# Kernel tuning notes

Hardware: AMD Instinct MI355X
Metric: run time of the kernel (lower is better)

## Reference

```python
import jax, jax.numpy as jnp
import numpy as np

E, N, D = 640000, 10000, 128  # edges, nodes, feature dim (edge=node=global=128)
H, O = 256, 128               # MLP hidden / output dims; concat dim = 4*D = 512


def setup_inputs() -> dict:
    key = jax.random.key(0)
    ks = jax.random.split(key, 7)
    return {
        "edge_attr": jax.random.normal(ks[0], (E, D), dtype=jnp.float32),
        "node_attr": jax.random.normal(ks[1], (N, D), dtype=jnp.float32),
        "global_attr": jax.random.normal(ks[2], (D,), dtype=jnp.float32),
        "senders": jax.random.randint(ks[3], (E,), 0, N),
        "receivers": jax.random.randint(ks[4], (E,), 0, N),
        "W1": jax.random.normal(ks[5], (4 * D, H), dtype=jnp.float32) / np.float32(np.sqrt(4 * D)),
        "b1": jnp.zeros((H,), dtype=jnp.float32),
        "W2": jax.random.normal(ks[6], (H, O), dtype=jnp.float32) / np.float32(np.sqrt(H)),
        "b2": jnp.zeros((O,), dtype=jnp.float32),
    }


def reference(edge_attr, node_attr, global_attr, senders, receivers, W1, b1, W2, b2):
    # Batched form of the per-edge Python loop:
    #   cat([e.data, e.receiver.data, e.sender.data, G.global_attribute.data]) -> updater MLP
    num_edges = edge_attr.shape[0]
    g = jnp.broadcast_to(global_attr, (num_edges, global_attr.shape[0]))  # [E, Dg]
    x = jnp.concatenate(
        [edge_attr, node_attr[receivers], node_attr[senders], g], axis=-1
    )  # [E, 4D]
    h = jax.nn.relu(x @ W1 + b1)  # [E, H]
    return h @ W2 + b2            # [E, O] : updated edge attributes
```

## Files before the change

### kernel.cpp

```cpp
#include <hip/hip_runtime.h>
#include <hip/hip_bf16.h>


typedef __attribute__((ext_vector_type(8))) short bf16x8;
typedef __attribute__((ext_vector_type(4))) float f32x4;
typedef __attribute__((ext_vector_type(2))) unsigned int u32x2;

static __device__ __forceinline__ unsigned short f2bf(float f) {
    unsigned u = __builtin_bit_cast(unsigned, f);
    u += 0x7FFFu + ((u >> 16) & 1u);
    return (unsigned short)(u >> 16);
}

static __device__ __forceinline__ unsigned cvt_pk_bf16(float lo, float hi) {
    unsigned r;
    asm("v_cvt_pk_bf16_f32 %0, %1, %2" : "=v"(r) : "v"(lo), "v"(hi));
    return r;
}

static __device__ __forceinline__ float bflo(unsigned u) {
    return __builtin_bit_cast(float, u << 16);
}
static __device__ __forceinline__ float bfhi(unsigned u) {
    return __builtin_bit_cast(float, u & 0xFFFF0000u);
}


__global__ void prep_w1_kernel(const float* __restrict__ W1,
                               ushort* __restrict__ w1f) {
    int id = blockIdx.x * 256 + threadIdx.x;
    if (id >= 16 * 12 * 64) return;
    int l = id & 63, blk = id >> 6;
    int ks = blk % 12, gnt = blk / 12;
    int n  = gnt * 16 + (l & 15);
    int k0 = ks * 32 + (l >> 4) * 8;
    ushort tmp[8];
    #pragma unroll
    for (int j = 0; j < 8; ++j) tmp[j] = f2bf(W1[(k0 + j) * 256 + n]);
    *(bf16x8*)&w1f[(size_t)id * 8] = *(bf16x8*)tmp;
}

__global__ void prep_w2_kernel(const float* __restrict__ W2,
                               ushort* __restrict__ w2f) {
    int id = blockIdx.x * 256 + threadIdx.x;
    if (id >= 8 * 8 * 64) return;
    int l = id & 63, blk = id >> 6;
    int ks = blk % 8, gnt = blk / 8;
    int n  = gnt * 16 + (l & 15);
    int k0 = ks * 32 + (l >> 4) * 8;
    ushort tmp[8];
    #pragma unroll
    for (int j = 0; j < 8; ++j) tmp[j] = f2bf(W2[(k0 + j) * 128 + n]);
    *(bf16x8*)&w2f[(size_t)id * 8] = *(bf16x8*)tmp;
}

__global__ void prep_hbias_kernel(const float* __restrict__ W1,
                                  const float* __restrict__ b1,
                                  const float* __restrict__ g,
                                  float* __restrict__ hbias) {
    int n = threadIdx.x;
    float acc = b1[n];
    for (int k = 0; k < 128; ++k) acc += g[k] * W1[(384 + k) * 256 + n];
    hbias[n] = acc;
}

__global__ __launch_bounds__(256) void prep_proj_kernel(
    const float* __restrict__ node_attr,
    const ushort* __restrict__ w1f,
    const float* __restrict__ hbias,
    ushort* __restrict__ Pr,
    ushort* __restrict__ Ps)
{
    __shared__ ushort Xn[64 * 128];

    const int t = threadIdx.x, l = t & 63, wn = t >> 6;
    const int base = blockIdx.x * 64;
    const int lr = l & 15, q = l >> 4, lk = q * 8;

    #pragma unroll
    for (int p = 0; p < 4; ++p) {
        int chunk = p * 256 + t;
        int r  = chunk >> 4;
        int c0 = (chunk & 15) * 8;
        int node = base + r; if (node >= 10000) node = 9999;
        const float4* src = (const float4*)(node_attr + (size_t)node * 128 + c0);
        float4 a = src[0];
        float4 b = src[1];
        uint4 uu = { cvt_pk_bf16(a.x, a.y), cvt_pk_bf16(a.z, a.w),
                     cvt_pk_bf16(b.x, b.y), cvt_pk_bf16(b.z, b.w) };
        *(bf16x8*)&Xn[r * 128 + (c0 ^ ((r & 7) << 3))] = __builtin_bit_cast(bf16x8, uu);
    }
    __syncthreads();

    #pragma unroll
    for (int s = 0; s < 2; ++s) {
        f32x4 acc[4][4];
        #pragma unroll
        for (int mt = 0; mt < 4; ++mt)
            #pragma unroll
            for (int nt = 0; nt < 4; ++nt)
                acc[mt][nt] = (f32x4){0.f, 0.f, 0.f, 0.f};

        #pragma unroll
        for (int ks = 0; ks < 4; ++ks) {
            bf16x8 B[4];
            #pragma unroll
            for (int nt = 0; nt < 4; ++nt)
                B[nt] = *(const bf16x8*)&w1f[
                    (size_t)(((wn * 4 + nt) * 12 + 4 + s * 4 + ks) * 64 + l) * 8];
            bf16x8 X[4];
            const int kk = ks * 32 + lk;
            #pragma unroll
            for (int mt = 0; mt < 4; ++mt) {
                const int row = mt * 16 + lr;
                X[mt] = *(const bf16x8*)&Xn[row * 128 + (kk ^ ((row & 7) << 3))];
            }
            #pragma unroll
            for (int mt = 0; mt < 4; ++mt)
                #pragma unroll
                for (int nt = 0; nt < 4; ++nt)
                    acc[mt][nt] = __builtin_amdgcn_mfma_f32_16x16x32_bf16(
                        B[nt], X[mt], acc[mt][nt], 0, 0, 0);
        }

        ushort* P = s ? Ps : Pr;
        #pragma unroll
        for (int nt = 0; nt < 4; ++nt) {
            const int F = wn * 64 + nt * 16 + q * 4;
            float4 hb4 = {0.f, 0.f, 0.f, 0.f};
            if (s == 0) hb4 = *(const float4*)&hbias[F];
            #pragma unroll
            for (int mt = 0; mt < 4; ++mt) {
                const int node = base + mt * 16 + lr;
                if (node < 10000) {
                    u32x2 w = { cvt_pk_bf16(acc[mt][nt][0] + hb4.x,
                                            acc[mt][nt][1] + hb4.y),
                                cvt_pk_bf16(acc[mt][nt][2] + hb4.z,
                                            acc[mt][nt][3] + hb4.w) };
                    *(u32x2*)&P[(size_t)node * 256 + F] = w;
                }
            }
        }
    }
}


__global__ __launch_bounds__(256, 3) void edge_mlp_kernel(
    const float* __restrict__ edge_attr,
    const int* __restrict__ senders,
    const int* __restrict__ receivers,
    const ushort* __restrict__ w1f,
    const ushort* __restrict__ w2f,
    const ushort* __restrict__ Pr,
    const ushort* __restrict__ Ps,
    const float* __restrict__ b2,
    float* __restrict__ out)
{
    __shared__ ushort Xe[64 * 128];
    __shared__ ushort Hs[64 * 256];

    const int t    = threadIdx.x;
    const int l    = t & 63;
    const int wid  = t >> 6;
    const int base = blockIdx.x * 64;

    const int lr = l & 15;
    const int q  = l >> 4;
    const int lk = q * 8;

    int pr_off[4], ps_off[4];
    #pragma unroll
    for (int mt = 0; mt < 4; ++mt) {
        int e = base + mt * 16 + lr;
        pr_off[mt] = receivers[e] * 256;
        ps_off[mt] = senders[e]   * 256;
    }

    #pragma unroll
    for (int p = 0; p < 4; ++p) {
        int chunk = p * 256 + t;
        int r  = chunk >> 4;
        int c0 = (chunk & 15) * 8;
        const float4* src = (const float4*)(edge_attr + (size_t)(base + r) * 128 + c0);
        float4 a = src[0];
        float4 b = src[1];
        uint4 uu = { cvt_pk_bf16(a.x, a.y), cvt_pk_bf16(a.z, a.w),
                     cvt_pk_bf16(b.x, b.y), cvt_pk_bf16(b.z, b.w) };
        *(bf16x8*)&Xe[r * 128 + (c0 ^ ((r & 7) << 3))] = __builtin_bit_cast(bf16x8, uu);
    }

    __syncthreads();

    f32x4 acc[4][4];
    #pragma unroll
    for (int mt = 0; mt < 4; ++mt)
        #pragma unroll
        for (int nt = 0; nt < 4; ++nt)
            acc[mt][nt] = (f32x4){0.f, 0.f, 0.f, 0.f};

    bf16x8 B[2][4];
    #pragma unroll
    for (int nt = 0; nt < 4; ++nt)
        B[0][nt] = *(const bf16x8*)&w1f[(size_t)(((wid * 4 + nt) * 12 + 0) * 64 + l) * 8];

    #pragma unroll
    for (int ks = 0; ks < 4; ++ks) {
        const int cur = ks & 1;
        if (ks < 3) {
            #pragma unroll
            for (int nt = 0; nt < 4; ++nt)
                B[cur ^ 1][nt] = *(const bf16x8*)&w1f[
                    (size_t)(((wid * 4 + nt) * 12 + (ks + 1)) * 64 + l) * 8];
        }
        bf16x8 X[4];
        const int kk = ks * 32 + lk;
        #pragma unroll
        for (int mt = 0; mt < 4; ++mt) {
            const int row = mt * 16 + lr;
            X[mt] = *(const bf16x8*)&Xe[row * 128 + (kk ^ ((row & 7) << 3))];
        }
        #pragma unroll
        for (int mt = 0; mt < 4; ++mt)
            #pragma unroll
            for (int nt = 0; nt < 4; ++nt)
                acc[mt][nt] = __builtin_amdgcn_mfma_f32_16x16x32_bf16(
                    B[cur][nt], X[mt], acc[mt][nt], 0, 0, 0);
    }

    u32x2 pg[4][4], sg[4][4];
    #pragma unroll
    for (int nt = 0; nt < 4; ++nt) {
        const int F = wid * 64 + nt * 16 + q * 4;
        #pragma unroll
        for (int mt = 0; mt < 4; ++mt) {
            pg[nt][mt] = *(const u32x2*)&Pr[pr_off[mt] + F];
            sg[nt][mt] = *(const u32x2*)&Ps[ps_off[mt] + F];
        }
    }

    #pragma unroll
    for (int nt = 0; nt < 4; ++nt) {
        const int F = wid * 64 + nt * 16 + q * 4;
        #pragma unroll
        for (int mt = 0; mt < 4; ++mt) {
            u32x2 p = pg[nt][mt], s = sg[nt][mt];
            float v0 = fmaxf(acc[mt][nt][0] + bflo(p.x) + bflo(s.x), 0.f);
            float v1 = fmaxf(acc[mt][nt][1] + bfhi(p.x) + bfhi(s.x), 0.f);
            float v2 = fmaxf(acc[mt][nt][2] + bflo(p.y) + bflo(s.y), 0.f);
            float v3 = fmaxf(acc[mt][nt][3] + bfhi(p.y) + bfhi(s.y), 0.f);
            u32x2 w = { cvt_pk_bf16(v0, v1), cvt_pk_bf16(v2, v3) };
            const int edge = mt * 16 + lr;
            *(u32x2*)&Hs[edge * 256 + (F ^ ((edge & 7) << 3))] = w;
        }
    }

    __syncthreads();

    f32x4 acc2[4][2];
    #pragma unroll
    for (int mt = 0; mt < 4; ++mt)
        #pragma unroll
        for (int nt = 0; nt < 2; ++nt)
            acc2[mt][nt] = (f32x4){0.f, 0.f, 0.f, 0.f};

    bf16x8 W2b[2][2];
    #pragma unroll
    for (int nt = 0; nt < 2; ++nt)
        W2b[0][nt] = *(const bf16x8*)&w2f[(size_t)(((wid * 2 + nt) * 8 + 0) * 64 + l) * 8];

    #pragma unroll
    for (int ks = 0; ks < 8; ++ks) {
        const int cur = ks & 1;
        if (ks < 7) {
            #pragma unroll
            for (int nt = 0; nt < 2; ++nt)
                W2b[cur ^ 1][nt] = *(const bf16x8*)&w2f[
                    (size_t)(((wid * 2 + nt) * 8 + (ks + 1)) * 64 + l) * 8];
        }
        bf16x8 Hfr[4];
        const int F = ks * 32 + lk;
        #pragma unroll
        for (int mt = 0; mt < 4; ++mt) {
            const int edge = mt * 16 + lr;
            Hfr[mt] = *(const bf16x8*)&Hs[edge * 256 + (F ^ ((edge & 7) << 3))];
        }
        #pragma unroll
        for (int mt = 0; mt < 4; ++mt)
            #pragma unroll
            for (int nt = 0; nt < 2; ++nt)
                acc2[mt][nt] = __builtin_amdgcn_mfma_f32_16x16x32_bf16(
                    W2b[cur][nt], Hfr[mt], acc2[mt][nt], 0, 0, 0);
    }

    #pragma unroll
    for (int nt = 0; nt < 2; ++nt) {
        const int F = wid * 32 + nt * 16 + q * 4;
        float4 b24 = *(const float4*)&b2[F];
        #pragma unroll
        for (int mt = 0; mt < 4; ++mt) {
            float4 o = { acc2[mt][nt][0] + b24.x, acc2[mt][nt][1] + b24.y,
                         acc2[mt][nt][2] + b24.z, acc2[mt][nt][3] + b24.w };
            *(float4*)&out[(size_t)(base + mt * 16 + lr) * 128 + F] = o;
        }
    }
}


extern "C" void kernel_launch(void* const* d_in, const int* in_sizes, int n_in,
                              void* d_out, int out_size, void* d_ws, size_t ws_size,
                              hipStream_t stream) {
    (void)in_sizes; (void)n_in; (void)out_size; (void)ws_size;

    const float* edge_attr   = (const float*)d_in[0];
    const float* node_attr   = (const float*)d_in[1];
    const float* global_attr = (const float*)d_in[2];
    const int*   senders     = (const int*)d_in[3];
    const int*   receivers   = (const int*)d_in[4];
    const float* W1          = (const float*)d_in[5];
    const float* b1          = (const float*)d_in[6];
    const float* W2          = (const float*)d_in[7];
    const float* b2          = (const float*)d_in[8];
    float* out = (float*)d_out;

    ushort* w1f   = (ushort*)d_ws;
    ushort* w2f   = (ushort*)((char*)d_ws + 196608);
    float*  hbias = (float*)((char*)d_ws + 262144);
    ushort* Pr    = (ushort*)((char*)d_ws + 263168);
    ushort* Ps    = (ushort*)((char*)d_ws + 5383168);

    hipLaunchKernelGGL(prep_w1_kernel,    dim3(48),  dim3(256), 0, stream, W1, w1f);
    hipLaunchKernelGGL(prep_w2_kernel,    dim3(16),  dim3(256), 0, stream, W2, w2f);
    hipLaunchKernelGGL(prep_hbias_kernel, dim3(1),   dim3(256), 0, stream, W1, b1, global_attr, hbias);
    hipLaunchKernelGGL(prep_proj_kernel,  dim3(157), dim3(256), 0, stream,
                       node_attr, w1f, hbias, Pr, Ps);

    hipLaunchKernelGGL(edge_mlp_kernel, dim3(10000), dim3(256), 0, stream,
                       edge_attr, senders, receivers, w1f, w2f, Pr, Ps, b2, out);
}
```

Baseline: 312.6 us.

## Make edge MLP kernel persistent with register-prefetched next-tile edge data

Replaces the one-block-per-tile launch of 10000 blocks with a persistent grid of 768 blocks looping over tiles. Each block prefetches the next tile's edge features and sender/receiver indices into registers while computing the current tile, and writes them to LDS after the first GEMM. This is meant to hide global load latency and avoid per-block startup cost. In exchange, occupancy is lowered to 2 blocks per SM and register pressure rises.

Result: slower. 596.2 us (+90.7%).

```diff
diff --git a/kernel.cpp b/kernel.cpp
--- a/kernel.cpp
+++ b/kernel.cpp
@@ -5,6 +5,9 @@
 typedef __attribute__((ext_vector_type(8))) short bf16x8;
 typedef __attribute__((ext_vector_type(4))) float f32x4;
 typedef __attribute__((ext_vector_type(2))) unsigned int u32x2;
+
+#define NTILE 10000
+#define GRID  768
 
 static __device__ __forceinline__ unsigned short f2bf(float f) {
     unsigned u = __builtin_bit_cast(unsigned, f);
@@ -23,6 +26,13 @@
 }
 static __device__ __forceinline__ float bfhi(unsigned u) {
     return __builtin_bit_cast(float, u & 0xFFFF0000u);
+}
+
+static __device__ __forceinline__ void block_sync_lds() {
+    __builtin_amdgcn_sched_barrier(0);
+    asm volatile("s_waitcnt lgkmcnt(0)" ::: "memory");
+    __builtin_amdgcn_s_barrier();
+    __builtin_amdgcn_sched_barrier(0);
 }
 
 
@@ -82,7 +92,7 @@
         int chunk = p * 256 + t;
         int r  = chunk >> 4;
         int c0 = (chunk & 15) * 8;
-        int node = base + r; if (node >= 10000) node = 9999;
+        int node = base + r; if (node >= NTILE) node = NTILE - 1;
         const float4* src = (const float4*)(node_attr + (size_t)node * 128 + c0);
         float4 a = src[0];
         float4 b = src[1];
@@ -132,7 +142,7 @@
             #pragma unroll
             for (int mt = 0; mt < 4; ++mt) {
                 const int node = base + mt * 16 + lr;
-                if (node < 10000) {
+                if (node < NTILE) {
                     u32x2 w = { cvt_pk_bf16(acc[mt][nt][0] + hb4.x,
                                             acc[mt][nt][1] + hb4.y),
                                 cvt_pk_bf16(acc[mt][nt][2] + hb4.z,
@@ -145,7 +155,7 @@
 }
 
 
-__global__ __launch_bounds__(256, 3) void edge_mlp_kernel(
+__global__ __launch_bounds__(256, 2) void edge_mlp_kernel(
     const float* __restrict__ edge_attr,
     const int* __restrict__ senders,
     const int* __restrict__ receivers,
@@ -162,146 +172,197 @@
     const int t    = threadIdx.x;
     const int l    = t & 63;
     const int wid  = t >> 6;
-    const int base = blockIdx.x * 64;
-
     const int lr = l & 15;
     const int q  = l >> 4;
     const int lk = q * 8;
 
-    int pr_off[4], ps_off[4];
-    #pragma unroll
-    for (int mt = 0; mt < 4; ++mt) {
-        int e = base + mt * 16 + lr;
-        pr_off[mt] = receivers[e] * 256;
-        ps_off[mt] = senders[e]   * 256;
-    }
-
+    int sr[4], sc[4];
     #pragma unroll
     for (int p = 0; p < 4; ++p) {
         int chunk = p * 256 + t;
-        int r  = chunk >> 4;
-        int c0 = (chunk & 15) * 8;
-        const float4* src = (const float4*)(edge_attr + (size_t)(base + r) * 128 + c0);
-        float4 a = src[0];
-        float4 b = src[1];
-        uint4 uu = { cvt_pk_bf16(a.x, a.y), cvt_pk_bf16(a.z, a.w),
-                     cvt_pk_bf16(b.x, b.y), cvt_pk_bf16(b.z, b.w) };
-        *(bf16x8*)&Xe[r * 128 + (c0 ^ ((r & 7) << 3))] = __builtin_bit_cast(bf16x8, uu);
-    }
-
-    __syncthreads();
-
-    f32x4 acc[4][4];
-    #pragma unroll
-    for (int mt = 0; mt < 4; ++mt)
+        sr[p] = chunk >> 4;
+        sc[p] = (chunk & 15) * 8;
+    }
+
+    int ti = blockIdx.x;
+
+    int recvC[4], sendC[4], recvN[4], sendN[4];
+    #pragma unroll
+    for (int mt = 0; mt < 4; ++mt) {
+        int e = ti * 64 + mt * 16 + lr;
+        recvC[mt] = receivers[e];
+        sendC[mt] = senders[e];
+    }
+
+    float4 er[8];
+    #pragma unroll
+    for (int p = 0; p < 4; ++p) {
+        const float4* src = (const float4*)(edge_attr + (size_t)(ti * 64 + sr[p]) * 128 + sc[p]);
+        er[2 * p]     = src[0];
+        er[2 * p + 1] = src[1];
+    }
+    #pragma unroll
+    for (int p = 0; p < 4; ++p) {
+        uint4 uu = { cvt_pk_bf16(er[2*p].x, er[2*p].y),  cvt_pk_bf16(er[2*p].z, er[2*p].w),
+                     cvt_pk_bf16(er[2*p+1].x, er[2*p+1].y), cvt_pk_bf16(er[2*p+1].z, er[2*p+1].w) };
+        *(bf16x8*)&Xe[sr[p] * 128 + (sc[p] ^ ((sr[p] & 7) << 3))] = __builtin_bit_cast(bf16x8, uu);
+    }
+
+    int tn = ti + GRID; if (tn >= NTILE) tn = ti;
+    #pragma unroll
+    for (int p = 0; p < 4; ++p) {
+        const float4* src = (const float4*)(edge_attr + (size_t)(tn * 64 + sr[p]) * 128 + sc[p]);
+        er[2 * p]     = src[0];
+        er[2 * p + 1] = src[1];
+    }
+    #pragma unroll
+    for (int mt = 0; mt < 4; ++mt) {
+        int e = tn * 64 + mt * 16 + lr;
+        recvN[mt] = receivers[e];
+        sendN[mt] = senders[e];
+    }
+
+    block_sync_lds();
+
+    for (; ti < NTILE; ti += GRID) {
+        u32x2 pg[4][4], sg[4][4];
+        #pragma unroll
+        for (int nt = 0; nt < 4; ++nt) {
+            const int F = wid * 64 + nt * 16 + q * 4;
+            #pragma unroll
+            for (int mt = 0; mt < 4; ++mt) {
+                pg[nt][mt] = *(const u32x2*)&Pr[(size_t)recvC[mt] * 256 + F];
+                sg[nt][mt] = *(const u32x2*)&Ps[(size_t)sendC[mt] * 256 + F];
+            }
+        }
+
+        f32x4 acc[4][4];
+        #pragma unroll
+        for (int mt = 0; mt < 4; ++mt)
+            #pragma unroll
+            for (int nt = 0; nt < 4; ++nt)
+                acc[mt][nt] = (f32x4){0.f, 0.f, 0.f, 0.f};
+
+        bf16x8 B[2][4];
         #pragma unroll
         for (int nt = 0; nt < 4; ++nt)
-            acc[mt][nt] = (f32x4){0.f, 0.f, 0.f, 0.f};
-
-    bf16x8 B[2][4];
-    #pragma unroll
-    for (int nt = 0; nt < 4; ++nt)
-        B[0][nt] = *(const bf16x8*)&w1f[(size_t)(((wid * 4 + nt) * 12 + 0) * 64 + l) * 8];
-
-    #pragma unroll
-    for (int ks = 0; ks < 4; ++ks) {
-        const int cur = ks & 1;
-        if (ks < 3) {
-            #pragma unroll
-            for (int nt = 0; nt < 4; ++nt)
-                B[cur ^ 1][nt] = *(const bf16x8*)&w1f[
-                    (size_t)(((wid * 4 + nt) * 12 + (ks + 1)) * 64 + l) * 8];
-        }
-        bf16x8 X[4];
-        const int kk = ks * 32 + lk;
+            B[0][nt] = *(const bf16x8*)&w1f[(size_t)(((wid * 4 + nt) * 12 + 0) * 64 + l) * 8];
+
+        #pragma unroll
+        for (int ks = 0; ks < 4; ++ks) {
+            const int cur = ks & 1;
+            if (ks < 3) {
+                #pragma unroll
+                for (int nt = 0; nt < 4; ++nt)
+                    B[cur ^ 1][nt] = *(const bf16x8*)&w1f[
+                        (size_t)(((wid * 4 + nt) * 12 + (ks + 1)) * 64 + l) * 8];
+            }
+            bf16x8 X[4];
+            const int kk = ks * 32 + lk;
+            #pragma unroll
+            for (int mt = 0; mt < 4; ++mt) {
+                const int row = mt * 16 + lr;
+                X[mt] = *(const bf16x8*)&Xe[row * 128 + (kk ^ ((row & 7) << 3))];
+            }
+            #pragma unroll
+            for (int mt = 0; mt < 4; ++mt)
+                #pragma unroll
+                for (int nt = 0; nt < 4; ++nt)
+                    acc[mt][nt] = __builtin_amdgcn_mfma_f32_16x16x32_bf16(
+                        B[cur][nt], X[mt], acc[mt][nt], 0, 0, 0);
+        }
+
+        #pragma unroll
+        for (int nt = 0; nt < 4; ++nt) {
+            const int F = wid * 64 + nt * 16 + q * 4;
+            #pragma unroll
+            for (int mt = 0; mt < 4; ++mt) {
+                u32x2 p = pg[nt][mt], s = sg[nt][mt];
+                float v0 = fmaxf(acc[mt][nt][0] + bflo(p.x) + bflo(s.x), 0.f);
+                float v1 = fmaxf(acc[mt][nt][1] + bfhi(p.x) + bfhi(s.x), 0.f);
+                float v2 = fmaxf(acc[mt][nt][2] + bflo(p.y) + bflo(s.y), 0.f);
+                float v3 = fmaxf(acc[mt][nt][3] + bfhi(p.y) + bfhi(s.y), 0.f);
+                u32x2 w = { cvt_pk_bf16(v0, v1), cvt_pk_bf16(v2, v3) };
+                const int edge = mt * 16 + lr;
+                *(u32x2*)&Hs[edge * 256 + (F ^ ((edge & 7) << 3))] = w;
+            }
+        }
+
+        block_sync_lds();
+
+        #pragma unroll
+        for (int p = 0; p < 4; ++p) {
+            uint4 uu = { cvt_pk_bf16(er[2*p].x, er[2*p].y),  cvt_pk_bf16(er[2*p].z, er[2*p].w),
+                         cvt_pk_bf16(er[2*p+1].x, er[2*p+1].y), cvt_pk_bf16(er[2*p+1].z, er[2*p+1].w) };
+            *(bf16x8*)&Xe[sr[p] * 128 + (sc[p] ^ ((sr[p] & 7) << 3))] = __builtin_bit_cast(bf16x8, uu);
+        }
+
+        int tn2 = ti + 2 * GRID; if (tn2 >= NTILE) tn2 = tn;
+        #pragma unroll
+        for (int p = 0; p < 4; ++p) {
+            const float4* src = (const float4*)(edge_attr + (size_t)(tn2 * 64 + sr[p]) * 128 + sc[p]);
+            er[2 * p]     = src[0];
+            er[2 * p + 1] = src[1];
+        }
         #pragma unroll
         for (int mt = 0; mt < 4; ++mt) {
-            const int row = mt * 16 + lr;
-            X[mt] = *(const bf16x8*)&Xe[row * 128 + (kk ^ ((row & 7) << 3))];
-        }
+            recvC[mt] = recvN[mt];
+            sendC[mt] = sendN[mt];
+            int e = tn2 * 64 + mt * 16 + lr;
+            recvN[mt] = receivers[e];
+            sendN[mt] = senders[e];
+        }
+
+        f32x4 acc2[4][2];
         #pragma unroll
         for (int mt = 0; mt < 4; ++mt)
             #pragma unroll
-            for (int nt = 0; nt < 4; ++nt)
-                acc[mt][nt] = __builtin_amdgcn_mfma_f32_16x16x32_bf16(
-                    B[cur][nt], X[mt], acc[mt][nt], 0, 0, 0);
-    }
-
-    u32x2 pg[4][4], sg[4][4];
-    #pragma unroll
-    for (int nt = 0; nt < 4; ++nt) {
-        const int F = wid * 64 + nt * 16 + q * 4;
-        #pragma unroll
-        for (int mt = 0; mt < 4; ++mt) {
-            pg[nt][mt] = *(const u32x2*)&Pr[pr_off[mt] + F];
-            sg[nt][mt] = *(const u32x2*)&Ps[ps_off[mt] + F];
-        }
-    }
-
-    #pragma unroll
-    for (int nt = 0; nt < 4; ++nt) {
-        const int F = wid * 64 + nt * 16 + q * 4;
-        #pragma unroll
-        for (int mt = 0; mt < 4; ++mt) {
-            u32x2 p = pg[nt][mt], s = sg[nt][mt];
-            float v0 = fmaxf(acc[mt][nt][0] + bflo(p.x) + bflo(s.x), 0.f);
-            float v1 = fmaxf(acc[mt][nt][1] + bfhi(p.x) + bfhi(s.x), 0.f);
-            float v2 = fmaxf(acc[mt][nt][2] + bflo(p.y) + bflo(s.y), 0.f);
-            float v3 = fmaxf(acc[mt][nt][3] + bfhi(p.y) + bfhi(s.y), 0.f);
-            u32x2 w = { cvt_pk_bf16(v0, v1), cvt_pk_bf16(v2, v3) };
-            const int edge = mt * 16 + lr;
-            *(u32x2*)&Hs[edge * 256 + (F ^ ((edge & 7) << 3))] = w;
-        }
-    }
-
-    __syncthreads();
-
-    f32x4 acc2[4][2];
-    #pragma unroll
-    for (int mt = 0; mt < 4; ++mt)
+            for (int nt = 0; nt < 2; ++nt)
+                acc2[mt][nt] = (f32x4){0.f, 0.f, 0.f, 0.f};
+
+        bf16x8 W2b[2][2];
         #pragma unroll
         for (int nt = 0; nt < 2; ++nt)
-            acc2[mt][nt] = (f32x4){0.f, 0.f, 0.f, 0.f};
-
-    bf16x8 W2b[2][2];
-    #pragma unroll
-    for (int nt = 0; nt < 2; ++nt)
-        W2b[0][nt] = *(const bf16x8*)&w2f[(size_t)(((wid * 2 + nt) * 8 + 0) * 64 + l) * 8];
-
-    #pragma unroll
-    for (int ks = 0; ks < 8; ++ks) {
-        const int cur = ks & 1;
-        if (ks < 7) {
-            #pragma unroll
-            for (int nt = 0; nt < 2; ++nt)
-                W2b[cur ^ 1][nt] = *(const bf16x8*)&w2f[
-                    (size_t)(((wid * 2 + nt) * 8 + (ks + 1)) * 64 + l) * 8];
-        }
-        bf16x8 Hfr[4];
-        const int F = ks * 32 + lk;
-        #pragma unroll
-        for (int mt = 0; mt < 4; ++mt) {
-            const int edge = mt * 16 + lr;
-            Hfr[mt] = *(const bf16x8*)&Hs[edge * 256 + (F ^ ((edge & 7) << 3))];
-        }
-        #pragma unroll
-        for (int mt = 0; mt < 4; ++mt)
-            #pragma unroll
-            for (int nt = 0; nt < 2; ++nt)
-                acc2[mt][nt] = __builtin_amdgcn_mfma_f32_16x16x32_bf16(
-                    W2b[cur][nt], Hfr[mt], acc2[mt][nt], 0, 0, 0);
-    }
-
-    #pragma unroll
-    for (int nt = 0; nt < 2; ++nt) {
-        const int F = wid * 32 + nt * 16 + q * 4;
-        float4 b24 = *(const float4*)&b2[F];
-        #pragma unroll
-        for (int mt = 0; mt < 4; ++mt) {
-            float4 o = { acc2[mt][nt][0] + b24.x, acc2[mt][nt][1] + b24.y,
-                         acc2[mt][nt][2] + b24.z, acc2[mt][nt][3] + b24.w };
-            *(float4*)&out[(size_t)(base + mt * 16 + lr) * 128 + F] = o;
-        }
+            W2b[0][nt] = *(const bf16x8*)&w2f[(size_t)(((wid * 2 + nt) * 8 + 0) * 64 + l) * 8];
+
+        #pragma unroll
+        for (int ks = 0; ks < 8; ++ks) {
+            const int cur = ks & 1;
+            if (ks < 7) {
+                #pragma unroll
+                for (int nt = 0; nt < 2; ++nt)
+                    W2b[cur ^ 1][nt] = *(const bf16x8*)&w2f[
+                        (size_t)(((wid * 2 + nt) * 8 + (ks + 1)) * 64 + l) * 8];
+            }
+            bf16x8 Hfr[4];
+            const int F = ks * 32 + lk;
+            #pragma unroll
+            for (int mt = 0; mt < 4; ++mt) {
+                const int edge = mt * 16 + lr;
+                Hfr[mt] = *(const bf16x8*)&Hs[edge * 256 + (F ^ ((edge & 7) << 3))];
+            }
+            #pragma unroll
+            for (int mt = 0; mt < 4; ++mt)
+                #pragma unroll
+                for (int nt = 0; nt < 2; ++nt)
+                    acc2[mt][nt] = __builtin_amdgcn_mfma_f32_16x16x32_bf16(
+                        W2b[cur][nt], Hfr[mt], acc2[mt][nt], 0, 0, 0);
+        }
+
+        #pragma unroll
+        for (int nt = 0; nt < 2; ++nt) {
+            const int F = wid * 32 + nt * 16 + q * 4;
+            float4 b24 = *(const float4*)&b2[F];
+            #pragma unroll
+            for (int mt = 0; mt < 4; ++mt) {
+                float4 o = { acc2[mt][nt][0] + b24.x, acc2[mt][nt][1] + b24.y,
+                             acc2[mt][nt][2] + b24.z, acc2[mt][nt][3] + b24.w };
+                *(float4*)&out[(size_t)(ti * 64 + mt * 16 + lr) * 128 + F] = o;
+            }
+        }
+
+        tn = tn2;
+        block_sync_lds();
     }
 }
 
@@ -334,6 +395,6 @@
     hipLaunchKernelGGL(prep_proj_kernel,  dim3(157), dim3(256), 0, stream,
                        node_attr, w1f, hbias, Pr, Ps);
 
-    hipLaunchKernelGGL(edge_mlp_kernel, dim3(10000), dim3(256), 0, stream,
+    hipLaunchKernelGGL(edge_mlp_kernel, dim3(GRID), dim3(256), 0, stream,
                        edge_attr, senders, receivers, w1f, w2f, Pr, Ps, b2, out);
 }
```

## Make edge MLP persistent with async LDS staging and register-resident weights

Applied to the files above, without the earlier changes.

Turns the edge MLP into a persistent kernel of 256 blocks with 512 threads, each looping over 40 edge tiles. Edge attributes are staged as fp32 straight into double-buffered LDS with global_load_lds and converted to bf16 on read. Index loads and node-projection gathers are software-pipelined one to two tiles ahead. W1 and W2 fragments are held in registers for the whole kernel instead of being reloaded per tile. The aim is to hide gather and load latency and cut per-block setup, at the cost of much higher register and LDS pressure and hand-tuned vmcnt waits that are fragile if the load counts change.

Result: slower. 420.4 us (+34.5%).

```diff
diff --git a/kernel.cpp b/kernel.cpp
--- a/kernel.cpp
+++ b/kernel.cpp
@@ -5,6 +5,10 @@
 typedef __attribute__((ext_vector_type(8))) short bf16x8;
 typedef __attribute__((ext_vector_type(4))) float f32x4;
 typedef __attribute__((ext_vector_type(2))) unsigned int u32x2;
+
+#define NTILE 10000
+#define NBLK  256
+#define NITER 40
 
 static __device__ __forceinline__ unsigned short f2bf(float f) {
     unsigned u = __builtin_bit_cast(unsigned, f);
@@ -24,6 +28,16 @@
 static __device__ __forceinline__ float bfhi(unsigned u) {
     return __builtin_bit_cast(float, u & 0xFFFF0000u);
 }
+
+static __device__ __forceinline__ void block_sync_lds() {
+    __builtin_amdgcn_sched_barrier(0);
+    asm volatile("s_waitcnt lgkmcnt(0)" ::: "memory");
+    __builtin_amdgcn_s_barrier();
+    __builtin_amdgcn_sched_barrier(0);
+}
+
+typedef __attribute__((address_space(1))) const unsigned int ga_uint;
+typedef __attribute__((address_space(3))) unsigned int lds_uint;
 
 
 __global__ void prep_w1_kernel(const float* __restrict__ W1,
@@ -82,7 +96,7 @@
         int chunk = p * 256 + t;
         int r  = chunk >> 4;
         int c0 = (chunk & 15) * 8;
-        int node = base + r; if (node >= 10000) node = 9999;
+        int node = base + r; if (node >= NTILE) node = NTILE - 1;
         const float4* src = (const float4*)(node_attr + (size_t)node * 128 + c0);
         float4 a = src[0];
         float4 b = src[1];
@@ -132,7 +146,7 @@
             #pragma unroll
             for (int mt = 0; mt < 4; ++mt) {
                 const int node = base + mt * 16 + lr;
-                if (node < 10000) {
+                if (node < NTILE) {
                     u32x2 w = { cvt_pk_bf16(acc[mt][nt][0] + hb4.x,
                                             acc[mt][nt][1] + hb4.y),
                                 cvt_pk_bf16(acc[mt][nt][2] + hb4.z,
@@ -145,7 +159,7 @@
 }
 
 
-__global__ __launch_bounds__(256, 3) void edge_mlp_kernel(
+__global__ __launch_bounds__(512, 2) void edge_mlp_kernel(
     const float* __restrict__ edge_attr,
     const int* __restrict__ senders,
     const int* __restrict__ receivers,
@@ -156,152 +170,204 @@
     const float* __restrict__ b2,
     float* __restrict__ out)
 {
-    __shared__ ushort Xe[64 * 128];
+    __shared__ float  Xe[2][64 * 128];
     __shared__ ushort Hs[64 * 256];
 
-    const int t    = threadIdx.x;
-    const int l    = t & 63;
-    const int wid  = t >> 6;
-    const int base = blockIdx.x * 64;
-
+    const int t  = threadIdx.x;
+    const int l  = t & 63;
+    const int w  = t >> 6;
+    const int wm = w >> 2;
+    const int wn = w & 3;
     const int lr = l & 15;
     const int q  = l >> 4;
-    const int lk = q * 8;
-
-    int pr_off[4], ps_off[4];
-    #pragma unroll
-    for (int mt = 0; mt < 4; ++mt) {
-        int e = base + mt * 16 + lr;
-        pr_off[mt] = receivers[e] * 256;
-        ps_off[mt] = senders[e]   * 256;
+    const int b  = blockIdx.x;
+
+    bf16x8 W1r[4][4];
+    #pragma unroll
+    for (int nt = 0; nt < 4; ++nt)
+        #pragma unroll
+        for (int ks = 0; ks < 4; ++ks)
+            W1r[nt][ks] = *(const bf16x8*)&w1f[
+                (size_t)(((wn * 4 + nt) * 12 + ks) * 64 + l) * 8];
+    bf16x8 W2r[2][8];
+    #pragma unroll
+    for (int nt = 0; nt < 2; ++nt)
+        #pragma unroll
+        for (int ks = 0; ks < 8; ++ks)
+            W2r[nt][ks] = *(const bf16x8*)&w2f[
+                (size_t)(((wn * 2 + nt) * 8 + ks) * 64 + l) * 8];
+
+    float4 b2v[2];
+    #pragma unroll
+    for (int nt = 0; nt < 2; ++nt)
+        b2v[nt] = *(const float4*)&b2[wn * 32 + nt * 16 + q * 4];
+
+    int rcA[2], scA[2], rcB[2], scB[2];
+    u32x2 pgA[4][2], sgA[4][2], pgB[4][2], sgB[4][2];
+
+    auto tile_of = [&](int it) {
+        int v = b + it * NBLK;
+        return v < NTILE ? v : v - NTILE;
+    };
+
+    auto stage = [&](int tile, int buf) {
+        #pragma unroll
+        for (int i = 0; i < 4; ++i) {
+            int row = w * 8 + i * 2 + (l >> 5);
+            int gs  = (l & 31) ^ (row & 7);
+            const unsigned int* src = (const unsigned int*)(edge_attr
+                + (size_t)(tile * 64 + row) * 128) + gs * 4;
+            unsigned int* dst = (unsigned int*)&Xe[buf][0] + (w * 4 + i) * 256;
+            __builtin_amdgcn_global_load_lds((ga_uint*)src, (lds_uint*)dst, 16, 0, 0);
+        }
+        __builtin_amdgcn_sched_barrier(0);
+    };
+
+    auto ld_idx = [&](int tile, int (&rc)[2], int (&sc)[2]) {
+        #pragma unroll
+        for (int mt = 0; mt < 2; ++mt) {
+            int e = tile * 64 + wm * 32 + mt * 16 + lr;
+            rc[mt] = receivers[e];
+            sc[mt] = senders[e];
+        }
+        __builtin_amdgcn_sched_barrier(0);
+    };
+
+    auto gather = [&](const int (&rc)[2], const int (&sc)[2],
+                      u32x2 (&pg)[4][2], u32x2 (&sg)[4][2]) {
+        #pragma unroll
+        for (int nt = 0; nt < 4; ++nt) {
+            const int F = wn * 64 + nt * 16 + q * 4;
+            #pragma unroll
+            for (int mt = 0; mt < 2; ++mt) {
+                pg[nt][mt] = *(const u32x2*)&Pr[(size_t)rc[mt] * 256 + F];
+                sg[nt][mt] = *(const u32x2*)&Ps[(size_t)sc[mt] * 256 + F];
+            }
+        }
+        __builtin_amdgcn_sched_barrier(0);
+    };
+
+    {
+        int t0 = tile_of(0), t1 = tile_of(1);
+        stage(t0, 0);
+        ld_idx(t0, rcA, scA);
+        gather(rcA, scA, pgA, sgA);
+        stage(t1, 1);
+        ld_idx(t1, rcB, scB);
+        asm volatile("s_waitcnt vmcnt(28)" ::: "memory");
+        __builtin_amdgcn_sched_barrier(0);
+        __builtin_amdgcn_s_barrier();
+        __builtin_amdgcn_sched_barrier(0);
     }
 
-    #pragma unroll
-    for (int p = 0; p < 4; ++p) {
-        int chunk = p * 256 + t;
-        int r  = chunk >> 4;
-        int c0 = (chunk & 15) * 8;
-        const float4* src = (const float4*)(edge_attr + (size_t)(base + r) * 128 + c0);
-        float4 a = src[0];
-        float4 b = src[1];
-        uint4 uu = { cvt_pk_bf16(a.x, a.y), cvt_pk_bf16(a.z, a.w),
-                     cvt_pk_bf16(b.x, b.y), cvt_pk_bf16(b.z, b.w) };
-        *(bf16x8*)&Xe[r * 128 + (c0 ^ ((r & 7) << 3))] = __builtin_bit_cast(bf16x8, uu);
-    }
-
-    __syncthreads();
-
-    f32x4 acc[4][4];
-    #pragma unroll
-    for (int mt = 0; mt < 4; ++mt)
-        #pragma unroll
-        for (int nt = 0; nt < 4; ++nt)
-            acc[mt][nt] = (f32x4){0.f, 0.f, 0.f, 0.f};
-
-    bf16x8 B[2][4];
-    #pragma unroll
-    for (int nt = 0; nt < 4; ++nt)
-        B[0][nt] = *(const bf16x8*)&w1f[(size_t)(((wid * 4 + nt) * 12 + 0) * 64 + l) * 8];
-
-    #pragma unroll
-    for (int ks = 0; ks < 4; ++ks) {
-        const int cur = ks & 1;
-        if (ks < 3) {
+    auto body = [&](int it, int buf,
+                    int (&rcUse)[2], int (&scUse)[2],
+                    int (&rcLoad)[2], int (&scLoad)[2],
+                    u32x2 (&pgC)[4][2], u32x2 (&sgC)[4][2],
+                    u32x2 (&pgN)[4][2], u32x2 (&sgN)[4][2])
+    {
+        const int tc = tile_of(it);
+
+        ld_idx(tile_of(it + 2), rcLoad, scLoad);
+
+        f32x4 acc[2][4];
+        #pragma unroll
+        for (int mt = 0; mt < 2; ++mt)
             #pragma unroll
             for (int nt = 0; nt < 4; ++nt)
-                B[cur ^ 1][nt] = *(const bf16x8*)&w1f[
-                    (size_t)(((wid * 4 + nt) * 12 + (ks + 1)) * 64 + l) * 8];
-        }
-        bf16x8 X[4];
-        const int kk = ks * 32 + lk;
-        #pragma unroll
-        for (int mt = 0; mt < 4; ++mt) {
-            const int row = mt * 16 + lr;
-            X[mt] = *(const bf16x8*)&Xe[row * 128 + (kk ^ ((row & 7) << 3))];
-        }
-        #pragma unroll
-        for (int mt = 0; mt < 4; ++mt)
-            #pragma unroll
-            for (int nt = 0; nt < 4; ++nt)
-                acc[mt][nt] = __builtin_amdgcn_mfma_f32_16x16x32_bf16(
-                    B[cur][nt], X[mt], acc[mt][nt], 0, 0, 0);
-    }
-
-    u32x2 pg[4][4], sg[4][4];
-    #pragma unroll
-    for (int nt = 0; nt < 4; ++nt) {
-        const int F = wid * 64 + nt * 16 + q * 4;
-        #pragma unroll
-        for (int mt = 0; mt < 4; ++mt) {
-            pg[nt][mt] = *(const u32x2*)&Pr[pr_off[mt] + F];
-            sg[nt][mt] = *(const u32x2*)&Ps[ps_off[mt] + F];
-        }
-    }
-
-    #pragma unroll
-    for (int nt = 0; nt < 4; ++nt) {
-        const int F = wid * 64 + nt * 16 + q * 4;
-        #pragma unroll
-        for (int mt = 0; mt < 4; ++mt) {
-            u32x2 p = pg[nt][mt], s = sg[nt][mt];
-            float v0 = fmaxf(acc[mt][nt][0] + bflo(p.x) + bflo(s.x), 0.f);
-            float v1 = fmaxf(acc[mt][nt][1] + bfhi(p.x) + bfhi(s.x), 0.f);
-            float v2 = fmaxf(acc[mt][nt][2] + bflo(p.y) + bflo(s.y), 0.f);
-            float v3 = fmaxf(acc[mt][nt][3] + bfhi(p.y) + bfhi(s.y), 0.f);
-            u32x2 w = { cvt_pk_bf16(v0, v1), cvt_pk_bf16(v2, v3) };
-            const int edge = mt * 16 + lr;
-            *(u32x2*)&Hs[edge * 256 + (F ^ ((edge & 7) << 3))] = w;
-        }
-    }
-
-    __syncthreads();
-
-    f32x4 acc2[4][2];
-    #pragma unroll
-    for (int mt = 0; mt < 4; ++mt)
-        #pragma unroll
-        for (int nt = 0; nt < 2; ++nt)
-            acc2[mt][nt] = (f32x4){0.f, 0.f, 0.f, 0.f};
-
-    bf16x8 W2b[2][2];
-    #pragma unroll
-    for (int nt = 0; nt < 2; ++nt)
-        W2b[0][nt] = *(const bf16x8*)&w2f[(size_t)(((wid * 2 + nt) * 8 + 0) * 64 + l) * 8];
-
-    #pragma unroll
-    for (int ks = 0; ks < 8; ++ks) {
-        const int cur = ks & 1;
-        if (ks < 7) {
+                acc[mt][nt] = (f32x4){0.f, 0.f, 0.f, 0.f};
+
+        #pragma unroll
+        for (int ks = 0; ks < 4; ++ks) {
+            bf16x8 X[2];
+            #pragma unroll
+            for (int mt = 0; mt < 2; ++mt) {
+                const int edge = wm * 32 + mt * 16 + lr;
+                const int s0 = ks * 8 + q * 2;
+                const char* base = (const char*)&Xe[buf][0] + edge * 512;
+                float4 xa = *(const float4*)(base + (((s0)     ^ (edge & 7)) * 16));
+                float4 xb = *(const float4*)(base + (((s0 + 1) ^ (edge & 7)) * 16));
+                uint4 uu = { cvt_pk_bf16(xa.x, xa.y), cvt_pk_bf16(xa.z, xa.w),
+                             cvt_pk_bf16(xb.x, xb.y), cvt_pk_bf16(xb.z, xb.w) };
+                X[mt] = __builtin_bit_cast(bf16x8, uu);
+            }
+            #pragma unroll
+            for (int mt = 0; mt < 2; ++mt)
+                #pragma unroll
+                for (int nt = 0; nt < 4; ++nt)
+                    acc[mt][nt] = __builtin_amdgcn_mfma_f32_16x16x32_bf16(
+                        W1r[nt][ks], X[mt], acc[mt][nt], 0, 0, 0);
+        }
+
+        #pragma unroll
+        for (int nt = 0; nt < 4; ++nt) {
+            const int F = wn * 64 + nt * 16 + q * 4;
+            #pragma unroll
+            for (int mt = 0; mt < 2; ++mt) {
+                u32x2 p = pgC[nt][mt], s = sgC[nt][mt];
+                float v0 = fmaxf(acc[mt][nt][0] + bflo(p.x) + bflo(s.x), 0.f);
+                float v1 = fmaxf(acc[mt][nt][1] + bfhi(p.x) + bfhi(s.x), 0.f);
+                float v2 = fmaxf(acc[mt][nt][2] + bflo(p.y) + bflo(s.y), 0.f);
+                float v3 = fmaxf(acc[mt][nt][3] + bfhi(p.y) + bfhi(s.y), 0.f);
+                u32x2 wv = { cvt_pk_bf16(v0, v1), cvt_pk_bf16(v2, v3) };
+                const int edge = wm * 32 + mt * 16 + lr;
+                *(u32x2*)&Hs[edge * 256 + (F ^ ((edge & 7) << 3))] = wv;
+            }
+        }
+
+        gather(rcUse, scUse, pgN, sgN);
+
+        block_sync_lds();
+
+        stage(tile_of(it + 2), buf);
+
+        f32x4 acc2[2][2];
+        #pragma unroll
+        for (int mt = 0; mt < 2; ++mt)
             #pragma unroll
             for (int nt = 0; nt < 2; ++nt)
-                W2b[cur ^ 1][nt] = *(const bf16x8*)&w2f[
-                    (size_t)(((wid * 2 + nt) * 8 + (ks + 1)) * 64 + l) * 8];
-        }
-        bf16x8 Hfr[4];
-        const int F = ks * 32 + lk;
-        #pragma unroll
-        for (int mt = 0; mt < 4; ++mt) {
-            const int edge = mt * 16 + lr;
-            Hfr[mt] = *(const bf16x8*)&Hs[edge * 256 + (F ^ ((edge & 7) << 3))];
-        }
-        #pragma unroll
-        for (int mt = 0; mt < 4; ++mt)
-            #pragma unroll
-            for (int nt = 0; nt < 2; ++nt)
-                acc2[mt][nt] = __builtin_amdgcn_mfma_f32_16x16x32_bf16(
-                    W2b[cur][nt], Hfr[mt], acc2[mt][nt], 0, 0, 0);
-    }
-
-    #pragma unroll
-    for (int nt = 0; nt < 2; ++nt) {
-        const int F = wid * 32 + nt * 16 + q * 4;
-        float4 b24 = *(const float4*)&b2[F];
-        #pragma unroll
-        for (int mt = 0; mt < 4; ++mt) {
-            float4 o = { acc2[mt][nt][0] + b24.x, acc2[mt][nt][1] + b24.y,
-                         acc2[mt][nt][2] + b24.z, acc2[mt][nt][3] + b24.w };
-            *(float4*)&out[(size_t)(base + mt * 16 + lr) * 128 + F] = o;
-        }
+                acc2[mt][nt] = (f32x4){0.f, 0.f, 0.f, 0.f};
+
+        #pragma unroll
+        for (int ks = 0; ks < 8; ++ks) {
+            bf16x8 Hfr[2];
+            #pragma unroll
+            for (int mt = 0; mt < 2; ++mt) {
+                const int edge = wm * 32 + mt * 16 + lr;
+                const int F0 = ks * 32 + q * 8;
+                Hfr[mt] = *(const bf16x8*)&Hs[edge * 256 + (F0 ^ ((edge & 7) << 3))];
+            }
+            #pragma unroll
+            for (int mt = 0; mt < 2; ++mt)
+                #pragma unroll
+                for (int nt = 0; nt < 2; ++nt)
+                    acc2[mt][nt] = __builtin_amdgcn_mfma_f32_16x16x32_bf16(
+                        W2r[nt][ks], Hfr[mt], acc2[mt][nt], 0, 0, 0);
+        }
+
+        #pragma unroll
+        for (int nt = 0; nt < 2; ++nt) {
+            const int F = wn * 32 + nt * 16 + q * 4;
+            #pragma unroll
+            for (int mt = 0; mt < 2; ++mt) {
+                const int e = tc * 64 + wm * 32 + mt * 16 + lr;
+                float4 o = { acc2[mt][nt][0] + b2v[nt].x, acc2[mt][nt][1] + b2v[nt].y,
+                             acc2[mt][nt][2] + b2v[nt].z, acc2[mt][nt][3] + b2v[nt].w };
+                *(float4*)&out[(size_t)e * 128 + F] = o;
+            }
+        }
+        __builtin_amdgcn_sched_barrier(0);
+
+        asm volatile("s_waitcnt vmcnt(32)" ::: "memory");
+        __builtin_amdgcn_sched_barrier(0);
+        __builtin_amdgcn_s_barrier();
+        __builtin_amdgcn_sched_barrier(0);
+    };
+
+    #pragma unroll 1
+    for (int it = 0; it < NITER; it += 2) {
+        body(it,     0, rcB, scB, rcA, scA, pgA, sgA, pgB, sgB);
+        body(it + 1, 1, rcA, scA, rcB, scB, pgB, sgB, pgA, sgA);
     }
 }
 
@@ -334,6 +400,6 @@
     hipLaunchKernelGGL(prep_proj_kernel,  dim3(157), dim3(256), 0, stream,
                        node_attr, w1f, hbias, Pr, Ps);
 
-    hipLaunchKernelGGL(edge_mlp_kernel, dim3(10000), dim3(256), 0, stream,
+    hipLaunchKernelGGL(edge_mlp_kernel, dim3(NBLK), dim3(512), 0, stream,
                        edge_attr, senders, receivers, w1f, w2f, Pr, Ps, b2, out);
 }
```

## Give each wave its own 16-edge slice and load edge features directly to registers

Applied to the files above, without the earlier changes.

The edge MLP kernel is restructured so each wave owns 16 edges and computes all 256 hidden and 128 output features for them, instead of waves splitting the feature dimension across 64 shared edges. Edge features are loaded and converted straight into MFMA operand registers, which removes the Xe shared-memory tile and one block barrier. Gathered projections are now fetched before the first GEMM so their latency overlaps the MFMAs. In exchange each wave streams all of W1 and W2 from global/L2 with no double buffering, adding weight traffic per edge and register pressure (16 accumulators plus 32 gather registers).

New measurement: 442.0 us. 1.41x slower.

```diff
diff --git a/kernel.cpp b/kernel.cpp
--- a/kernel.cpp
+++ b/kernel.cpp
@@ -5,6 +5,8 @@
 typedef __attribute__((ext_vector_type(8))) short bf16x8;
 typedef __attribute__((ext_vector_type(4))) float f32x4;
 typedef __attribute__((ext_vector_type(2))) unsigned int u32x2;
+
+#define NTILE 10000
 
 static __device__ __forceinline__ unsigned short f2bf(float f) {
     unsigned u = __builtin_bit_cast(unsigned, f);
@@ -82,7 +84,7 @@
         int chunk = p * 256 + t;
         int r  = chunk >> 4;
         int c0 = (chunk & 15) * 8;
-        int node = base + r; if (node >= 10000) node = 9999;
+        int node = base + r; if (node >= NTILE) node = NTILE - 1;
         const float4* src = (const float4*)(node_attr + (size_t)node * 128 + c0);
         float4 a = src[0];
         float4 b = src[1];
@@ -132,7 +134,7 @@
             #pragma unroll
             for (int mt = 0; mt < 4; ++mt) {
                 const int node = base + mt * 16 + lr;
-                if (node < 10000) {
+                if (node < NTILE) {
                     u32x2 w = { cvt_pk_bf16(acc[mt][nt][0] + hb4.x,
                                             acc[mt][nt][1] + hb4.y),
                                 cvt_pk_bf16(acc[mt][nt][2] + hb4.z,
@@ -156,152 +158,89 @@
     const float* __restrict__ b2,
     float* __restrict__ out)
 {
-    __shared__ ushort Xe[64 * 128];
     __shared__ ushort Hs[64 * 256];
 
-    const int t    = threadIdx.x;
-    const int l    = t & 63;
-    const int wid  = t >> 6;
-    const int base = blockIdx.x * 64;
-
+    const int t  = threadIdx.x;
+    const int l  = t & 63;
+    const int w  = t >> 6;
     const int lr = l & 15;
     const int q  = l >> 4;
-    const int lk = q * 8;
-
-    int pr_off[4], ps_off[4];
-    #pragma unroll
-    for (int mt = 0; mt < 4; ++mt) {
-        int e = base + mt * 16 + lr;
-        pr_off[mt] = receivers[e] * 256;
-        ps_off[mt] = senders[e]   * 256;
-    }
-
-    #pragma unroll
-    for (int p = 0; p < 4; ++p) {
-        int chunk = p * 256 + t;
-        int r  = chunk >> 4;
-        int c0 = (chunk & 15) * 8;
-        const float4* src = (const float4*)(edge_attr + (size_t)(base + r) * 128 + c0);
-        float4 a = src[0];
-        float4 b = src[1];
-        uint4 uu = { cvt_pk_bf16(a.x, a.y), cvt_pk_bf16(a.z, a.w),
-                     cvt_pk_bf16(b.x, b.y), cvt_pk_bf16(b.z, b.w) };
-        *(bf16x8*)&Xe[r * 128 + (c0 ^ ((r & 7) << 3))] = __builtin_bit_cast(bf16x8, uu);
+    const int row  = w * 16 + lr;
+    const size_t ebase = (size_t)blockIdx.x * 64 + w * 16;
+
+    const int rc = receivers[ebase + lr];
+    const int sc = senders[ebase + lr];
+
+    const float* erow = edge_attr + (ebase + lr) * 128;
+    bf16x8 X[4];
+    #pragma unroll
+    for (int ks = 0; ks < 4; ++ks) {
+        float4 xa = *(const float4*)(erow + ks * 32 + q * 8);
+        float4 xb = *(const float4*)(erow + ks * 32 + q * 8 + 4);
+        uint4 uu = { cvt_pk_bf16(xa.x, xa.y), cvt_pk_bf16(xa.z, xa.w),
+                     cvt_pk_bf16(xb.x, xb.y), cvt_pk_bf16(xb.z, xb.w) };
+        X[ks] = __builtin_bit_cast(bf16x8, uu);
+    }
+
+    u32x2 pg[16], sg[16];
+    #pragma unroll
+    for (int nt = 0; nt < 16; ++nt) {
+        const int F = nt * 16 + q * 4;
+        pg[nt] = *(const u32x2*)&Pr[(size_t)rc * 256 + F];
+        sg[nt] = *(const u32x2*)&Ps[(size_t)sc * 256 + F];
+    }
+
+    f32x4 acc[16];
+    #pragma unroll
+    for (int nt = 0; nt < 16; ++nt)
+        acc[nt] = (f32x4){0.f, 0.f, 0.f, 0.f};
+
+    #pragma unroll
+    for (int ks = 0; ks < 4; ++ks)
+        #pragma unroll
+        for (int nt = 0; nt < 16; ++nt) {
+            bf16x8 Wf = *(const bf16x8*)&w1f[(size_t)((nt * 12 + ks) * 64 + l) * 8];
+            acc[nt] = __builtin_amdgcn_mfma_f32_16x16x32_bf16(Wf, X[ks], acc[nt], 0, 0, 0);
+        }
+
+    #pragma unroll
+    for (int nt = 0; nt < 16; ++nt) {
+        u32x2 p = pg[nt], s = sg[nt];
+        float v0 = fmaxf(acc[nt][0] + bflo(p.x) + bflo(s.x), 0.f);
+        float v1 = fmaxf(acc[nt][1] + bfhi(p.x) + bfhi(s.x), 0.f);
+        float v2 = fmaxf(acc[nt][2] + bflo(p.y) + bflo(s.y), 0.f);
+        float v3 = fmaxf(acc[nt][3] + bfhi(p.y) + bfhi(s.y), 0.f);
+        u32x2 wv = { cvt_pk_bf16(v0, v1), cvt_pk_bf16(v2, v3) };
+        const int F = nt * 16 + q * 4;
+        *(u32x2*)&Hs[row * 256 + (F ^ ((row & 7) << 3))] = wv;
     }
 
     __syncthreads();
 
-    f32x4 acc[4][4];
-    #pragma unroll
-    for (int mt = 0; mt < 4; ++mt)
-        #pragma unroll
-        for (int nt = 0; nt < 4; ++nt)
-            acc[mt][nt] = (f32x4){0.f, 0.f, 0.f, 0.f};
-
-    bf16x8 B[2][4];
-    #pragma unroll
-    for (int nt = 0; nt < 4; ++nt)
-        B[0][nt] = *(const bf16x8*)&w1f[(size_t)(((wid * 4 + nt) * 12 + 0) * 64 + l) * 8];
-
-    #pragma unroll
-    for (int ks = 0; ks < 4; ++ks) {
-        const int cur = ks & 1;
-        if (ks < 3) {
-            #pragma unroll
-            for (int nt = 0; nt < 4; ++nt)
-                B[cur ^ 1][nt] = *(const bf16x8*)&w1f[
-                    (size_t)(((wid * 4 + nt) * 12 + (ks + 1)) * 64 + l) * 8];
-        }
-        bf16x8 X[4];
-        const int kk = ks * 32 + lk;
-        #pragma unroll
-        for (int mt = 0; mt < 4; ++mt) {
-            const int row = mt * 16 + lr;
-            X[mt] = *(const bf16x8*)&Xe[row * 128 + (kk ^ ((row & 7) << 3))];
-        }
-        #pragma unroll
-        for (int mt = 0; mt < 4; ++mt)
-            #pragma unroll
-            for (int nt = 0; nt < 4; ++nt)
-                acc[mt][nt] = __builtin_amdgcn_mfma_f32_16x16x32_bf16(
-                    B[cur][nt], X[mt], acc[mt][nt], 0, 0, 0);
-    }
-
-    u32x2 pg[4][4], sg[4][4];
-    #pragma unroll
-    for (int nt = 0; nt < 4; ++nt) {
-        const int F = wid * 64 + nt * 16 + q * 4;
-        #pragma unroll
-        for (int mt = 0; mt < 4; ++mt) {
-            pg[nt][mt] = *(const u32x2*)&Pr[pr_off[mt] + F];
-            sg[nt][mt] = *(const u32x2*)&Ps[ps_off[mt] + F];
-        }
-    }
-
-    #pragma unroll
-    for (int nt = 0; nt < 4; ++nt) {
-        const int F = wid * 64 + nt * 16 + q * 4;
-        #pragma unroll
-        for (int mt = 0; mt < 4; ++mt) {
-            u32x2 p = pg[nt][mt], s = sg[nt][mt];
-            float v0 = fmaxf(acc[mt][nt][0] + bflo(p.x) + bflo(s.x), 0.f);
-            float v1 = fmaxf(acc[mt][nt][1] + bfhi(p.x) + bfhi(s.x), 0.f);
-            float v2 = fmaxf(acc[mt][nt][2] + bflo(p.y) + bflo(s.y), 0.f);
-            float v3 = fmaxf(acc[mt][nt][3] + bfhi(p.y) + bfhi(s.y), 0.f);
-            u32x2 w = { cvt_pk_bf16(v0, v1), cvt_pk_bf16(v2, v3) };
-            const int edge = mt * 16 + lr;
-            *(u32x2*)&Hs[edge * 256 + (F ^ ((edge & 7) << 3))] = w;
-        }
-    }
-
-    __syncthreads();
-
-    f32x4 acc2[4][2];
-    #pragma unroll
-    for (int mt = 0; mt < 4; ++mt)
-        #pragma unroll
-        for (int nt = 0; nt < 2; ++nt)
-            acc2[mt][nt] = (f32x4){0.f, 0.f, 0.f, 0.f};
-
-    bf16x8 W2b[2][2];
-    #pragma unroll
-    for (int nt = 0; nt < 2; ++nt)
-        W2b[0][nt] = *(const bf16x8*)&w2f[(size_t)(((wid * 2 + nt) * 8 + 0) * 64 + l) * 8];
+    f32x4 acc2[8];
+    #pragma unroll
+    for (int nt = 0; nt < 8; ++nt)
+        acc2[nt] = (f32x4){0.f, 0.f, 0.f, 0.f};
 
     #pragma unroll
     for (int ks = 0; ks < 8; ++ks) {
-        const int cur = ks & 1;
-        if (ks < 7) {
-            #pragma unroll
-            for (int nt = 0; nt < 2; ++nt)
-                W2b[cur ^ 1][nt] = *(const bf16x8*)&w2f[
-                    (size_t)(((wid * 2 + nt) * 8 + (ks + 1)) * 64 + l) * 8];
-        }
-        bf16x8 Hfr[4];
-        const int F = ks * 32 + lk;
-        #pragma unroll
-        for (int mt = 0; mt < 4; ++mt) {
-            const int edge = mt * 16 + lr;
-            Hfr[mt] = *(const bf16x8*)&Hs[edge * 256 + (F ^ ((edge & 7) << 3))];
-        }
-        #pragma unroll
-        for (int mt = 0; mt < 4; ++mt)
-            #pragma unroll
-            for (int nt = 0; nt < 2; ++nt)
-                acc2[mt][nt] = __builtin_amdgcn_mfma_f32_16x16x32_bf16(
-                    W2b[cur][nt], Hfr[mt], acc2[mt][nt], 0, 0, 0);
-    }
-
-    #pragma unroll
-    for (int nt = 0; nt < 2; ++nt) {
-        const int F = wid * 32 + nt * 16 + q * 4;
+        const int F0 = ks * 32 + q * 8;
+        bf16x8 Hf = *(const bf16x8*)&Hs[row * 256 + (F0 ^ ((row & 7) << 3))];
+        #pragma unroll
+        for (int nt = 0; nt < 8; ++nt) {
+            bf16x8 Wf = *(const bf16x8*)&w2f[(size_t)((nt * 8 + ks) * 64 + l) * 8];
+            acc2[nt] = __builtin_amdgcn_mfma_f32_16x16x32_bf16(Wf, Hf, acc2[nt], 0, 0, 0);
+        }
+    }
+
+    float* orow = out + (ebase + lr) * 128;
+    #pragma unroll
+    for (int nt = 0; nt < 8; ++nt) {
+        const int F = nt * 16 + q * 4;
         float4 b24 = *(const float4*)&b2[F];
-        #pragma unroll
-        for (int mt = 0; mt < 4; ++mt) {
-            float4 o = { acc2[mt][nt][0] + b24.x, acc2[mt][nt][1] + b24.y,
-                         acc2[mt][nt][2] + b24.z, acc2[mt][nt][3] + b24.w };
-            *(float4*)&out[(size_t)(base + mt * 16 + lr) * 128 + F] = o;
-        }
+        float4 o = { acc2[nt][0] + b24.x, acc2[nt][1] + b24.y,
+                     acc2[nt][2] + b24.z, acc2[nt][3] + b24.w };
+        *(float4*)(orow + F) = o;
     }
 }
 
```
